# Kernel optimization log

Hardware: AMD Instinct MI355X
Metric: run time of the kernel (lower is better)

The kernel has to match this reference:

```python
import jax, jax.numpy as jnp
import numpy as np

D_MODEL = 1024
NUM_HEADS = 16
HEAD_DIM = D_MODEL // NUM_HEADS
SCALE = HEAD_DIM ** -0.5
ROPE_BASE = 10000.0


def _rope_cos_sin(seq_len, dim, dtype=jnp.float32):
    inv_freq = 1.0 / (ROPE_BASE ** (jnp.arange(0, dim, 2, dtype=jnp.float32) / dim))
    t = jnp.arange(seq_len, dtype=jnp.float32)
    freqs = t[:, None] * inv_freq[None, :]            # [S, dim/2]
    emb = jnp.concatenate([freqs, freqs], axis=-1)    # [S, dim]
    # broadcast shape [1, S, 1, dim] to apply over [B, S, H, dim]
    return emb.astype(dtype)[None, :, None, :]


def _rotate_half(x):
    half = x.shape[-1] // 2
    x1, x2 = x[..., :half], x[..., half:]
    return jnp.concatenate([-x2, x1], axis=-1)


def setup_inputs() -> dict:
    key = jax.random.key(0)
    ks = jax.random.split(key, 5)
    B, S = 2, 2048
    x = jax.random.normal(ks[0], (B, S, D_MODEL), dtype=jnp.float32)
    wq = jax.random.normal(ks[1], (D_MODEL, D_MODEL), dtype=jnp.float32) * (D_MODEL ** -0.5)
    wk = jax.random.normal(ks[2], (D_MODEL, D_MODEL), dtype=jnp.float32) * (D_MODEL ** -0.5)
    wv = jax.random.normal(ks[3], (D_MODEL, D_MODEL), dtype=jnp.float32) * (D_MODEL ** -0.5)
    wo = jax.random.normal(ks[4], (D_MODEL, D_MODEL), dtype=jnp.float32) * (D_MODEL ** -0.5)
    attention_mask = jnp.tril(jnp.ones((S, S), dtype=jnp.int32))  # causal
    return {"x": x, "wq": wq, "wk": wk, "wv": wv, "wo": wo,
            "attention_mask": attention_mask}


def reference(x, wq, wk, wv, wo, attention_mask):
    B, S, _ = x.shape
    # projections (nn.Linear, no bias: y = x @ W^T)
    q = (x @ wq.T).reshape(B, S, NUM_HEADS, HEAD_DIM)
    k = (x @ wk.T).reshape(B, S, NUM_HEADS, HEAD_DIM)
    v = (x @ wv.T).reshape(B, S, NUM_HEADS, HEAD_DIM)
    # RoPE
    emb = _rope_cos_sin(S, HEAD_DIM, x.dtype)
    cos, sin = jnp.cos(emb), jnp.sin(emb)
    q = q * cos + _rotate_half(q) * sin
    k = k * cos + _rotate_half(k) * sin
    # attention scores [B, H, S, S]
    scores = jnp.einsum('bihd,bjhd->bhij', q, k) * SCALE
    mask = attention_mask[None, None, :, :]  # 2D mask -> broadcast over batch, heads
    scores = jnp.where(mask == 0, -jnp.inf, scores)
    attn = jax.nn.softmax(scores, axis=-1)
    attn = jnp.nan_to_num(attn, nan=0.0)  # fully-masked rows -> 0
    out = jnp.einsum('bhij,bjhd->bihd', attn, v).reshape(B, S, D_MODEL)
    return out @ wo.T
```

## Files before the change

kernel.cpp:

```cpp
#include <hip/hip_runtime.h>

typedef __bf16 bf16;
typedef __attribute__((ext_vector_type(8))) __bf16 bf16x8;
typedef __attribute__((ext_vector_type(4))) float f32x4;
typedef __attribute__((ext_vector_type(4))) short s16x4;
typedef __attribute__((ext_vector_type(4))) unsigned u32x4;

#define SEQ 2048
#define DM 1024
#define NH 16
#define HD 64
#define QSCALE 0.1803368801111204f

static __device__ __forceinline__ void gl_lds16(const bf16* g, bf16* l) {
  __builtin_amdgcn_global_load_lds(
      (const __attribute__((address_space(1))) void*)g,
      (__attribute__((address_space(3))) void*)l, 16, 0, 0);
}

static __device__ __forceinline__ f32x4 mfma16(bf16x8 a, bf16x8 b, f32x4 c) {
  return __builtin_amdgcn_mfma_f32_16x16x32_bf16(a, b, c, 0, 0, 0);
}

static __device__ __forceinline__ unsigned cvt_pk_bf16(float lo, float hi) {
  unsigned r;
  asm("v_cvt_pk_bf16_f32 %0, %1, %2" : "=v"(r) : "v"(lo), "v"(hi));
  return r;
}

static __device__ __forceinline__ float vmax4(f32x4 v) {
  return fmaxf(fmaxf(v[0], v[1]), fmaxf(v[2], v[3]));
}

__global__ __launch_bounds__(256)
void prep_k(const float* __restrict__ x, const float* __restrict__ wq,
            const float* __restrict__ wk, const float* __restrict__ wv,
            const float* __restrict__ wo, bf16* __restrict__ xb,
            bf16* __restrict__ wb, float* __restrict__ tab) {
  int i = blockIdx.x * 256 + threadIdx.x;
  if (i < 2097152) {
    const float* src;
    bf16* dst;
    int j;
    if (i < 1048576) {
      src = x; dst = xb; j = i;
    } else {
      j = i - 1048576;
      int seg = j >> 18;
      src = (seg == 0) ? wq : (seg == 1) ? wk : (seg == 2) ? wv : wo;
      dst = wb;
      src -= (size_t)seg << 20;
    }
    f32x4 v = ((const f32x4*)src)[j];
    s16x4 o;
#pragma unroll
    for (int q = 0; q < 4; ++q) o[q] = __builtin_bit_cast(short, (bf16)v[q]);
    ((s16x4*)dst)[j] = o;
  } else {
    int idx = i - 2097152;
    int s = idx >> 5, j = idx & 31;
    float inv = powf(10000.0f, -(float)j * (1.0f / 32.0f));
    float f = (float)s * inv;
    tab[idx * 2] = cosf(f);
    tab[idx * 2 + 1] = sinf(f);
  }
}

__global__ __launch_bounds__(256)
void gemm_qkv(const bf16* __restrict__ A, const bf16* __restrict__ B,
              bf16* __restrict__ qh, bf16* __restrict__ kh, bf16* __restrict__ vt,
              const float2* __restrict__ tab) {
  const int K = 1024;
  __shared__ __attribute__((aligned(16))) bf16 As[128 * 32];
  __shared__ __attribute__((aligned(16))) bf16 Bs[128 * 32];
  const int t = threadIdx.x;
  const int wv = t >> 6, ln = t & 63, lr = ln & 15, lg = ln >> 4;
  const int wr = wv >> 1, wc = wv & 1;
  const int m0 = blockIdx.y * 128, n0 = blockIdx.x * 128;
  const int srow = t >> 2, sslot = t & 3;
  const int seg = n0 >> 10;
  const int hh = ((n0 & 1023) + wc * 64) >> 6;

  f32x4 acc[4][4] = {};

  for (int kt = 0; kt < K; kt += 32) {
#pragma unroll
    for (int c = 0; c < 2; ++c) {
      int row = srow + (c << 6);
      int lsl = sslot ^ (row & 3);
      gl_lds16(A + (size_t)(m0 + row) * K + kt + lsl * 8, As + c * 2048 + wv * 512);
      gl_lds16(B + (size_t)(n0 + row) * K + kt + lsl * 8, Bs + c * 2048 + wv * 512);
    }
    __syncthreads();
    bf16x8 af[4], bfr[4];
#pragma unroll
    for (int i = 0; i < 4; ++i) {
      int ra = wr * 64 + i * 16 + lr;
      af[i] = *(const bf16x8*)(As + ra * 32 + ((lg ^ (ra & 3)) << 3));
      int rb = wc * 64 + i * 16 + lr;
      bfr[i] = *(const bf16x8*)(Bs + rb * 32 + ((lg ^ (rb & 3)) << 3));
    }
#pragma unroll
    for (int i = 0; i < 4; ++i)
#pragma unroll
      for (int j = 0; j < 4; ++j)
        acc[i][j] = mfma16(af[i], bfr[j], acc[i][j]);
    __syncthreads();
  }

#pragma unroll
  for (int i = 0; i < 4; ++i) {
    int row0 = m0 + wr * 64 + i * 16 + lg * 4;
    int bb = row0 >> 11, s0r = row0 & (SEQ - 1);
    if (seg < 2) {
      bf16* dst = (seg == 0) ? qh : kh;
      float scl = (seg == 0) ? QSCALE : 1.0f;
      size_t base = ((size_t)(bb * NH + hh) * SEQ + s0r) * HD;
#pragma unroll
      for (int j = 0; j < 2; ++j) {
        int dlo = j * 16 + lr;
#pragma unroll
        for (int r = 0; r < 4; ++r) {
          float2 cs = tab[(size_t)(s0r + r) * 32 + dlo];
          float a = acc[i][j][r], b2 = acc[i][j + 2][r];
          float na = (a * cs.x - b2 * cs.y) * scl;
          float nb = (b2 * cs.x + a * cs.y) * scl;
          dst[base + (size_t)r * HD + dlo] = (bf16)na;
          dst[base + (size_t)r * HD + dlo + 32] = (bf16)nb;
        }
      }
    } else {
#pragma unroll
      for (int j = 0; j < 4; ++j) {
        int d = j * 16 + lr;
        s16x4 pk;
#pragma unroll
        for (int r = 0; r < 4; ++r) pk[r] = __builtin_bit_cast(short, (bf16)acc[i][j][r]);
        *(s16x4*)(vt + ((size_t)(bb * NH + hh) * HD + d) * SEQ + s0r) = pk;
      }
    }
  }
}

__global__ __launch_bounds__(256)
void gemm_bt_f32(const bf16* __restrict__ A, const bf16* __restrict__ B,
                 float* __restrict__ C, int M, int N, int K) {
  __shared__ __attribute__((aligned(16))) bf16 As[128 * 32];
  __shared__ __attribute__((aligned(16))) bf16 Bs[128 * 32];
  const int t = threadIdx.x;
  const int wv = t >> 6, ln = t & 63, lr = ln & 15, lg = ln >> 4;
  const int wr = wv >> 1, wc = wv & 1;
  const int m0 = blockIdx.y * 128, n0 = blockIdx.x * 128;
  const int srow = t >> 2, sslot = t & 3;

  f32x4 acc[4][4] = {};

  for (int kt = 0; kt < K; kt += 32) {
#pragma unroll
    for (int c = 0; c < 2; ++c) {
      int row = srow + (c << 6);
      int lsl = sslot ^ (row & 3);
      gl_lds16(A + (size_t)(m0 + row) * K + kt + lsl * 8, As + c * 2048 + wv * 512);
      gl_lds16(B + (size_t)(n0 + row) * K + kt + lsl * 8, Bs + c * 2048 + wv * 512);
    }
    __syncthreads();
    bf16x8 af[4], bfr[4];
#pragma unroll
    for (int i = 0; i < 4; ++i) {
      int ra = wr * 64 + i * 16 + lr;
      af[i] = *(const bf16x8*)(As + ra * 32 + ((lg ^ (ra & 3)) << 3));
      int rb = wc * 64 + i * 16 + lr;
      bfr[i] = *(const bf16x8*)(Bs + rb * 32 + ((lg ^ (rb & 3)) << 3));
    }
#pragma unroll
    for (int i = 0; i < 4; ++i)
#pragma unroll
      for (int j = 0; j < 4; ++j)
        acc[i][j] = mfma16(af[i], bfr[j], acc[i][j]);
    __syncthreads();
  }

#pragma unroll
  for (int i = 0; i < 4; ++i) {
    int row0 = m0 + wr * 64 + i * 16 + lg * 4;
#pragma unroll
    for (int j = 0; j < 4; ++j) {
      int col = n0 + wc * 64 + j * 16 + lr;
#pragma unroll
      for (int r = 0; r < 4; ++r)
        C[(size_t)(row0 + r) * N + col] = acc[i][j][r];
    }
  }
}

template <bool MASKED>
static __device__ __forceinline__ void attn_tile_lds(
    const bf16* Ksb, const bf16* Vsb, unsigned* plw,
    const bf16x8* qf, f32x4* acc, float& m_run, float& l_run,
    int lr, int lg, int qrow, int s0) {
  f32x4 sc[4] = {};
#pragma unroll
  for (int fi = 0; fi < 4; ++fi) {
    int row = fi * 16 + lr;
    int sw = row & 7;
    bf16x8 k0 = *(const bf16x8*)(Ksb + row * 64 + ((lg ^ sw) << 3));
    bf16x8 k1 = *(const bf16x8*)(Ksb + row * 64 + (((4 + lg) ^ sw) << 3));
    sc[fi] = mfma16(k0, qf[0], sc[fi]);
    sc[fi] = mfma16(k1, qf[1], sc[fi]);
  }
  if (MASKED) {
#pragma unroll
    for (int fi = 0; fi < 4; ++fi)
#pragma unroll
      for (int r = 0; r < 4; ++r) {
        int kv = s0 + fi * 16 + lg * 4 + r;
        sc[fi][r] = (kv <= qrow) ? sc[fi][r] : -3e38f;
      }
  }
  float mx = fmaxf(fmaxf(vmax4(sc[0]), vmax4(sc[1])),
                   fmaxf(vmax4(sc[2]), vmax4(sc[3])));
  mx = fmaxf(mx, __shfl_xor(mx, 16));
  mx = fmaxf(mx, __shfl_xor(mx, 32));
  if (!__all(mx <= m_run)) {
    float mn = fmaxf(m_run, mx);
    float alpha = __builtin_amdgcn_exp2f(m_run - mn);
    m_run = mn;
    l_run *= alpha;
#pragma unroll
    for (int d0 = 0; d0 < 4; ++d0)
#pragma unroll
      for (int r = 0; r < 4; ++r) acc[d0][r] *= alpha;
  }
  float pf[4][4], sm = 0.0f;
#pragma unroll
  for (int fi = 0; fi < 4; ++fi)
#pragma unroll
    for (int r = 0; r < 4; ++r) {
      pf[fi][r] = __builtin_amdgcn_exp2f(sc[fi][r] - m_run);
      sm += pf[fi][r];
    }
  sm += __shfl_xor(sm, 16);
  sm += __shfl_xor(sm, 32);
  l_run += sm;

  const int sw2 = (lr & 7) << 2;
#pragma unroll
  for (int fi = 0; fi < 4; ++fi)
#pragma unroll
    for (int hh = 0; hh < 2; ++hh)
      plw[lr * 32 + ((fi * 8 + lg * 2 + hh) ^ sw2)] =
          cvt_pk_bf16(pf[fi][2 * hh], pf[fi][2 * hh + 1]);
  asm volatile("s_waitcnt lgkmcnt(0)" ::: "memory");
  __builtin_amdgcn_sched_barrier(0);
#pragma unroll
  for (int kc = 0; kc < 2; ++kc) {
    u32x4 praw = *(const u32x4*)(plw + lr * 32 + ((kc * 16 + lg * 4) ^ sw2));
    bf16x8 pb = __builtin_bit_cast(bf16x8, praw);
#pragma unroll
    for (int d0 = 0; d0 < 4; ++d0) {
      int row = d0 * 16 + lr;
      int sw = row & 7;
      bf16x8 vf = *(const bf16x8*)(Vsb + row * 64 + (((kc * 4 + lg) ^ sw) << 3));
      acc[d0] = mfma16(vf, pb, acc[d0]);
    }
  }
  asm volatile("" ::: "memory");
}

__global__ __launch_bounds__(256, 4)
void attn_k(const bf16* __restrict__ qh, const bf16* __restrict__ kh,
            const bf16* __restrict__ vt, bf16* __restrict__ ao) {
  __shared__ __attribute__((aligned(16))) bf16 Ks[2][64 * 64];
  __shared__ __attribute__((aligned(16))) bf16 Vs[2][64 * 64];
  __shared__ __attribute__((aligned(16))) unsigned plds[4][512];

  const int t = threadIdx.x, wv = t >> 6, ln = t & 63, lr = ln & 15, lg = ln >> 4;
  const int bid = blockIdx.x;
  const int xcd = bid & 7, g = bid >> 3;
  const int bh = xcd * 4 + (g & 3);
  const int qt = 31 - (g >> 2);
  const int b = bh >> 4, h = bh & 15;

  const bf16* qp = qh + (size_t)bh * SEQ * HD;
  const bf16* kp = kh + (size_t)bh * SEQ * HD;
  const bf16* vp = vt + (size_t)bh * HD * SEQ;
  unsigned* plw = &plds[wv][0];

  const int qrow = qt * 64 + wv * 16 + lr;

  bf16x8 qf[2];
  qf[0] = *(const bf16x8*)(qp + (size_t)qrow * HD + lg * 8);
  qf[1] = *(const bf16x8*)(qp + (size_t)qrow * HD + 32 + lg * 8);

  f32x4 acc[4] = {};
  float m_run = -3e38f, l_run = 0.0f;

  const int nt = qt + 1;

  auto STAGE = [&](int buf, int tt) {
    int s0 = tt * 64;
#pragma unroll
    for (int c = 0; c < 2; ++c) {
      int rA = wv * 16 + c * 8;
      int row = rA + (ln >> 3);
      int sl = (ln & 7) ^ (row & 7);
      gl_lds16(kp + (size_t)(s0 + row) * HD + (sl << 3), &Ks[buf][rA * 64]);
      gl_lds16(vp + (size_t)row * SEQ + s0 + (sl << 3), &Vs[buf][rA * 64]);
    }
  };

  STAGE(0, 0);
  asm volatile("s_waitcnt vmcnt(0)" ::: "memory");
  __builtin_amdgcn_s_barrier();

  int cur = 0;
  for (int tt = 0; tt < nt; ++tt) {
    if (tt + 1 < nt) STAGE(cur ^ 1, tt + 1);
    if (tt == qt)
      attn_tile_lds<true>(&Ks[cur][0], &Vs[cur][0], plw, qf, acc, m_run, l_run,
                          lr, lg, qrow, tt * 64);
    else
      attn_tile_lds<false>(&Ks[cur][0], &Vs[cur][0], plw, qf, acc, m_run, l_run,
                           lr, lg, qrow, tt * 64);
    asm volatile("s_waitcnt vmcnt(0)" ::: "memory");
    __builtin_amdgcn_s_barrier();
    cur ^= 1;
  }

  float invl = 1.0f / l_run;
  bf16* aop = ao + ((size_t)b * SEQ + qrow) * DM + h * HD;
#pragma unroll
  for (int d0 = 0; d0 < 4; ++d0) {
    unsigned lo = cvt_pk_bf16(acc[d0][0] * invl, acc[d0][1] * invl);
    unsigned hi = cvt_pk_bf16(acc[d0][2] * invl, acc[d0][3] * invl);
    uint2 pk; pk.x = lo; pk.y = hi;
    *(uint2*)(aop + d0 * 16 + lg * 4) = pk;
  }
}

extern "C" void kernel_launch(void* const* d_in, const int* in_sizes, int n_in,
                              void* d_out, int out_size, void* d_ws, size_t ws_size,
                              hipStream_t stream) {
  const float* x = (const float*)d_in[0];
  const float* wq = (const float*)d_in[1];
  const float* wk = (const float*)d_in[2];
  const float* wv = (const float*)d_in[3];
  const float* wo = (const float*)d_in[4];

  char* ws = (char*)d_ws;
  const size_t MB = 1ull << 20;
  bf16* xb    = (bf16*)ws;
  bf16* wqkvb = (bf16*)(ws + 8 * MB);
  bf16* wob   = (bf16*)(ws + 14 * MB);
  bf16* qhb   = (bf16*)(ws + 16 * MB);
  bf16* khb   = (bf16*)(ws + 24 * MB);
  bf16* vtb   = (bf16*)(ws + 32 * MB);
  float* tab  = (float*)(ws + 40 * MB);
  bf16* aob = xb;

  prep_k<<<8448, 256, 0, stream>>>(x, wq, wk, wv, wo, xb, wqkvb, tab);

  gemm_qkv<<<dim3(24, 32), 256, 0, stream>>>(xb, wqkvb, qhb, khb, vtb, (const float2*)tab);

  attn_k<<<1024, 256, 0, stream>>>(qhb, khb, vtb, aob);

  gemm_bt_f32<<<dim3(8, 32), 256, 0, stream>>>(aob, wob, (float*)d_out, 4096, 1024, 1024);
}
```

Before: 119.4 us.

## Rewrite attention as single-wave 32x32 MFMA blocks with register-resident K/V

```diff
diff --git a/kernel.cpp b/kernel.cpp
--- a/kernel.cpp
+++ b/kernel.cpp
@@ -3,6 +3,7 @@
 typedef __bf16 bf16;
 typedef __attribute__((ext_vector_type(8))) __bf16 bf16x8;
 typedef __attribute__((ext_vector_type(4))) float f32x4;
+typedef __attribute__((ext_vector_type(16))) float f32x16;
 typedef __attribute__((ext_vector_type(4))) short s16x4;
 typedef __attribute__((ext_vector_type(4))) unsigned u32x4;
 
@@ -21,15 +22,17 @@
 static __device__ __forceinline__ f32x4 mfma16(bf16x8 a, bf16x8 b, f32x4 c) {
   return __builtin_amdgcn_mfma_f32_16x16x32_bf16(a, b, c, 0, 0, 0);
 }
+static __device__ __forceinline__ f32x16 mfma32(bf16x8 a, bf16x8 b, f32x16 c) {
+  return __builtin_amdgcn_mfma_f32_32x32x16_bf16(a, b, c, 0, 0, 0);
+}
 
 static __device__ __forceinline__ unsigned cvt_pk_bf16(float lo, float hi) {
   unsigned r;
   asm("v_cvt_pk_bf16_f32 %0, %1, %2" : "=v"(r) : "v"(lo), "v"(hi));
   return r;
 }
-
-static __device__ __forceinline__ float vmax4(f32x4 v) {
-  return fmaxf(fmaxf(v[0], v[1]), fmaxf(v[2], v[3]));
+static __device__ __forceinline__ void pl32swap(unsigned& a, unsigned& b) {
+  asm("v_permlane32_swap_b32 %0, %1" : "+v"(a), "+v"(b));
 }
 
 __global__ __launch_bounds__(256)
@@ -193,148 +196,119 @@
   }
 }
 
-template <bool MASKED>
-static __device__ __forceinline__ void attn_tile_lds(
-    const bf16* Ksb, const bf16* Vsb, unsigned* plw,
-    const bf16x8* qf, f32x4* acc, float& m_run, float& l_run,
-    int lr, int lg, int qrow, int s0) {
-  f32x4 sc[4] = {};
-#pragma unroll
-  for (int fi = 0; fi < 4; ++fi) {
-    int row = fi * 16 + lr;
-    int sw = row & 7;
-    bf16x8 k0 = *(const bf16x8*)(Ksb + row * 64 + ((lg ^ sw) << 3));
-    bf16x8 k1 = *(const bf16x8*)(Ksb + row * 64 + (((4 + lg) ^ sw) << 3));
-    sc[fi] = mfma16(k0, qf[0], sc[fi]);
-    sc[fi] = mfma16(k1, qf[1], sc[fi]);
-  }
-  if (MASKED) {
-#pragma unroll
-    for (int fi = 0; fi < 4; ++fi)
-#pragma unroll
-      for (int r = 0; r < 4; ++r) {
-        int kv = s0 + fi * 16 + lg * 4 + r;
-        sc[fi][r] = (kv <= qrow) ? sc[fi][r] : -3e38f;
-      }
-  }
-  float mx = fmaxf(fmaxf(vmax4(sc[0]), vmax4(sc[1])),
-                   fmaxf(vmax4(sc[2]), vmax4(sc[3])));
-  mx = fmaxf(mx, __shfl_xor(mx, 16));
-  mx = fmaxf(mx, __shfl_xor(mx, 32));
-  if (!__all(mx <= m_run)) {
-    float mn = fmaxf(m_run, mx);
-    float alpha = __builtin_amdgcn_exp2f(m_run - mn);
-    m_run = mn;
-    l_run *= alpha;
-#pragma unroll
-    for (int d0 = 0; d0 < 4; ++d0)
-#pragma unroll
-      for (int r = 0; r < 4; ++r) acc[d0][r] *= alpha;
-  }
-  float pf[4][4], sm = 0.0f;
-#pragma unroll
-  for (int fi = 0; fi < 4; ++fi)
-#pragma unroll
-    for (int r = 0; r < 4; ++r) {
-      pf[fi][r] = __builtin_amdgcn_exp2f(sc[fi][r] - m_run);
-      sm += pf[fi][r];
-    }
-  sm += __shfl_xor(sm, 16);
-  sm += __shfl_xor(sm, 32);
-  l_run += sm;
-
-  const int sw2 = (lr & 7) << 2;
-#pragma unroll
-  for (int fi = 0; fi < 4; ++fi)
-#pragma unroll
-    for (int hh = 0; hh < 2; ++hh)
-      plw[lr * 32 + ((fi * 8 + lg * 2 + hh) ^ sw2)] =
-          cvt_pk_bf16(pf[fi][2 * hh], pf[fi][2 * hh + 1]);
-  asm volatile("s_waitcnt lgkmcnt(0)" ::: "memory");
-  __builtin_amdgcn_sched_barrier(0);
-#pragma unroll
-  for (int kc = 0; kc < 2; ++kc) {
-    u32x4 praw = *(const u32x4*)(plw + lr * 32 + ((kc * 16 + lg * 4) ^ sw2));
-    bf16x8 pb = __builtin_bit_cast(bf16x8, praw);
-#pragma unroll
-    for (int d0 = 0; d0 < 4; ++d0) {
-      int row = d0 * 16 + lr;
-      int sw = row & 7;
-      bf16x8 vf = *(const bf16x8*)(Vsb + row * 64 + (((kc * 4 + lg) ^ sw) << 3));
-      acc[d0] = mfma16(vf, pb, acc[d0]);
-    }
-  }
-  asm volatile("" ::: "memory");
-}
-
-__global__ __launch_bounds__(256, 4)
+__global__ __launch_bounds__(64, 3)
 void attn_k(const bf16* __restrict__ qh, const bf16* __restrict__ kh,
             const bf16* __restrict__ vt, bf16* __restrict__ ao) {
-  __shared__ __attribute__((aligned(16))) bf16 Ks[2][64 * 64];
-  __shared__ __attribute__((aligned(16))) bf16 Vs[2][64 * 64];
-  __shared__ __attribute__((aligned(16))) unsigned plds[4][512];
-
-  const int t = threadIdx.x, wv = t >> 6, ln = t & 63, lr = ln & 15, lg = ln >> 4;
+  const int l = threadIdx.x, q32 = l & 31, h5 = l >> 5;
   const int bid = blockIdx.x;
   const int xcd = bid & 7, g = bid >> 3;
   const int bh = xcd * 4 + (g & 3);
-  const int qt = 31 - (g >> 2);
+  const int qi = 63 - (g >> 2);
   const int b = bh >> 4, h = bh & 15;
-
-  const bf16* qp = qh + (size_t)bh * SEQ * HD;
-  const bf16* kp = kh + (size_t)bh * SEQ * HD;
-  const bf16* vp = vt + (size_t)bh * HD * SEQ;
-  unsigned* plw = &plds[wv][0];
-
-  const int qrow = qt * 64 + wv * 16 + lr;
-
-  bf16x8 qf[2];
-  qf[0] = *(const bf16x8*)(qp + (size_t)qrow * HD + lg * 8);
-  qf[1] = *(const bf16x8*)(qp + (size_t)qrow * HD + 32 + lg * 8);
-
-  f32x4 acc[4] = {};
+  const int nt = qi + 1;
+  const int qrow = qi * 32 + q32;
+
+  const bf16* qp = qh + ((size_t)bh * SEQ + qrow) * HD + h5 * 8;
+  const bf16* kp = kh + ((size_t)bh * SEQ + q32) * HD + h5 * 8;
+  const bf16* vp = vt + ((size_t)bh * HD + q32) * SEQ + h5 * 8;
+
+  bf16x8 qf[4];
+#pragma unroll
+  for (int ks = 0; ks < 4; ++ks) qf[ks] = *(const bf16x8*)(qp + ks * 16);
+
+  f32x16 acc0 = {}, acc1 = {};
   float m_run = -3e38f, l_run = 0.0f;
 
-  const int nt = qt + 1;
-
-  auto STAGE = [&](int buf, int tt) {
-    int s0 = tt * 64;
-#pragma unroll
-    for (int c = 0; c < 2; ++c) {
-      int rA = wv * 16 + c * 8;
-      int row = rA + (ln >> 3);
-      int sl = (ln & 7) ^ (row & 7);
-      gl_lds16(kp + (size_t)(s0 + row) * HD + (sl << 3), &Ks[buf][rA * 64]);
-      gl_lds16(vp + (size_t)row * SEQ + s0 + (sl << 3), &Vs[buf][rA * 64]);
-    }
+  bf16x8 kfA[4], vfA[4], kfB[4], vfB[4];
+
+  auto LOAD = [&](bf16x8* kf, bf16x8* vf, int tt) {
+    const bf16* kt = kp + (size_t)tt * 32 * HD;
+#pragma unroll
+    for (int ks = 0; ks < 4; ++ks)
+      kf[ks] = *(const bf16x8*)(kt + ks * 16);
+#pragma unroll
+    for (int dh = 0; dh < 2; ++dh)
+#pragma unroll
+      for (int k2 = 0; k2 < 2; ++k2)
+        vf[dh * 2 + k2] = *(const bf16x8*)(vp + (size_t)dh * 32 * SEQ + tt * 32 + k2 * 16);
   };
 
-  STAGE(0, 0);
-  asm volatile("s_waitcnt vmcnt(0)" ::: "memory");
-  __builtin_amdgcn_s_barrier();
-
-  int cur = 0;
-  for (int tt = 0; tt < nt; ++tt) {
-    if (tt + 1 < nt) STAGE(cur ^ 1, tt + 1);
-    if (tt == qt)
-      attn_tile_lds<true>(&Ks[cur][0], &Vs[cur][0], plw, qf, acc, m_run, l_run,
-                          lr, lg, qrow, tt * 64);
-    else
-      attn_tile_lds<false>(&Ks[cur][0], &Vs[cur][0], plw, qf, acc, m_run, l_run,
-                           lr, lg, qrow, tt * 64);
-    asm volatile("s_waitcnt vmcnt(0)" ::: "memory");
-    __builtin_amdgcn_s_barrier();
-    cur ^= 1;
+  auto COMPUTE = [&](bf16x8* kf, bf16x8* vf, int tt, bool masked) {
+    f32x16 sc = {};
+#pragma unroll
+    for (int ks = 0; ks < 4; ++ks) sc = mfma32(kf[ks], qf[ks], sc);
+    if (masked) {
+#pragma unroll
+      for (int r = 0; r < 16; ++r) {
+        int kv = tt * 32 + (r & 3) + 8 * (r >> 2) + 4 * h5;
+        sc[r] = (kv <= qrow) ? sc[r] : -3e38f;
+      }
+    }
+    float mx = sc[0];
+#pragma unroll
+    for (int r = 1; r < 16; ++r) mx = fmaxf(mx, sc[r]);
+    mx = fmaxf(mx, __shfl_xor(mx, 32));
+    if (!__all(mx <= m_run)) {
+      float mn = fmaxf(m_run, mx);
+      float alpha = __builtin_amdgcn_exp2f(m_run - mn);
+      m_run = mn;
+      l_run *= alpha;
+#pragma unroll
+      for (int r = 0; r < 16; ++r) { acc0[r] *= alpha; acc1[r] *= alpha; }
+    }
+    float p[16], sm = 0.0f;
+#pragma unroll
+    for (int r = 0; r < 16; ++r) {
+      p[r] = __builtin_amdgcn_exp2f(sc[r] - m_run);
+      sm += p[r];
+    }
+    sm += __shfl_xor(sm, 32);
+    l_run += sm;
+    unsigned w[8];
+#pragma unroll
+    for (int j = 0; j < 8; ++j) w[j] = cvt_pk_bf16(p[2 * j], p[2 * j + 1]);
+    pl32swap(w[0], w[2]);
+    pl32swap(w[1], w[3]);
+    pl32swap(w[4], w[6]);
+    pl32swap(w[5], w[7]);
+    u32x4 u0 = {w[0], w[1], w[2], w[3]};
+    u32x4 u1 = {w[4], w[5], w[6], w[7]};
+    bf16x8 pb0 = __builtin_bit_cast(bf16x8, u0);
+    bf16x8 pb1 = __builtin_bit_cast(bf16x8, u1);
+    acc0 = mfma32(vf[0], pb0, acc0);
+    acc0 = mfma32(vf[1], pb1, acc0);
+    acc1 = mfma32(vf[2], pb0, acc1);
+    acc1 = mfma32(vf[3], pb1, acc1);
+  };
+
+  LOAD(kfA, vfA, 0);
+  int tt = 0;
+  for (;;) {
+    if (tt + 1 < nt) LOAD(kfB, vfB, tt + 1);
+    if (tt == nt - 1) { COMPUTE(kfA, vfA, tt, true); break; }
+    COMPUTE(kfA, vfA, tt, false);
+    ++tt;
+    if (tt + 1 < nt) LOAD(kfA, vfA, tt + 1);
+    if (tt == nt - 1) { COMPUTE(kfB, vfB, tt, true); break; }
+    COMPUTE(kfB, vfB, tt, false);
+    ++tt;
   }
 
   float invl = 1.0f / l_run;
   bf16* aop = ao + ((size_t)b * SEQ + qrow) * DM + h * HD;
 #pragma unroll
-  for (int d0 = 0; d0 < 4; ++d0) {
-    unsigned lo = cvt_pk_bf16(acc[d0][0] * invl, acc[d0][1] * invl);
-    unsigned hi = cvt_pk_bf16(acc[d0][2] * invl, acc[d0][3] * invl);
-    uint2 pk; pk.x = lo; pk.y = hi;
-    *(uint2*)(aop + d0 * 16 + lg * 4) = pk;
+  for (int dh = 0; dh < 2; ++dh) {
+#pragma unroll
+    for (int rq = 0; rq < 4; ++rq) {
+      float a0 = (dh ? acc1[4 * rq + 0] : acc0[4 * rq + 0]) * invl;
+      float a1 = (dh ? acc1[4 * rq + 1] : acc0[4 * rq + 1]) * invl;
+      float a2 = (dh ? acc1[4 * rq + 2] : acc0[4 * rq + 2]) * invl;
+      float a3 = (dh ? acc1[4 * rq + 3] : acc0[4 * rq + 3]) * invl;
+      uint2 pk2;
+      pk2.x = cvt_pk_bf16(a0, a1);
+      pk2.y = cvt_pk_bf16(a2, a3);
+      *(uint2*)(aop + dh * 32 + 8 * rq + 4 * h5) = pk2;
+    }
   }
 }
 
@@ -362,7 +336,7 @@
 
   gemm_qkv<<<dim3(24, 32), 256, 0, stream>>>(xb, wqkvb, qhb, khb, vtb, (const float2*)tab);
 
-  attn_k<<<1024, 256, 0, stream>>>(qhb, khb, vtb, aob);
+  attn_k<<<2048, 64, 0, stream>>>(qhb, khb, vtb, aob);
 
   gemm_bt_f32<<<dim3(8, 32), 256, 0, stream>>>(aob, wob, (float*)d_out, 4096, 1024, 1024);
 }
```

Measured after the change: 237.0 us. +98.5%, slower.
